# Kernel optimization log

Measured on AMD Instinct MI355X. Metric: run time of the kernel, lower is better.

## Reference

```python
import jax, jax.numpy as jnp
import numpy as np
import math

D_MODEL = 2048
K = 64
W = 512              # window_size
STRIDE = W // 2      # = 256
EMA_ALPHA = 0.9
N_RETRIEVE = 8
EPS = 1e-12


def _build_cheby(k, w):
    # cheby_mat[k, n] = cos(k * arccos(t_n)), t_n = cos(pi*(2n+1)/(2w))
    ns = np.arange(w, dtype=np.float64)
    t = np.cos(np.pi * (2 * ns + 1) / (2 * w))
    ks = np.arange(k, dtype=np.float64)
    return jnp.asarray(np.cos(ks[:, None] * np.arccos(t)[None, :]), dtype=jnp.float32)


def setup_inputs() -> dict:
    key = jax.random.key(0)
    ks = jax.random.split(key, 5)
    B, S = 2, 8192
    scan_out = jax.random.normal(ks[0], (B, S, D_MODEL), dtype=jnp.float32)
    buf = jax.random.normal(ks[1], (W, D_MODEL), dtype=jnp.float32)  # pre-filled circular buffer
    # unit-modulus random-phase complex roles: r_k[d] = exp(i*theta)
    phases = jax.random.uniform(ks[2], (K, D_MODEL), dtype=jnp.float32) * (2.0 * math.pi)
    roles_real = jnp.cos(phases)
    roles_imag = jnp.sin(phases)
    w_bands = 1.0 / (jnp.arange(K, dtype=jnp.float32) + 1.0)  # w_init = 1/(k+1)
    retrieve_proj_w = jax.random.normal(ks[3], (D_MODEL, D_MODEL), dtype=jnp.float32) * 0.02
    inject_gate = jnp.zeros((1,), dtype=jnp.float32)
    cheby_mat = _build_cheby(K, W)
    return dict(scan_out=scan_out, buf=buf, roles_real=roles_real, roles_imag=roles_imag,
                w_bands=w_bands, retrieve_proj_w=retrieve_proj_w, inject_gate=inject_gate,
                cheby_mat=cheby_mat)


def reference(scan_out, buf, roles_real, roles_imag, w_bands, retrieve_proj_w, inject_gate, cheby_mat):
    S = scan_out.shape[1]
    h_mean = scan_out.mean(axis=0)                      # [S, D] batch-mean like torch code
    n_chunks = S // STRIDE
    chunks = h_mean.reshape(n_chunks, STRIDE, D_MODEL)  # each chunk triggers one bind

    init = (buf, jnp.int32(0),
            jnp.zeros((K, D_MODEL), jnp.float32),   # c_past
            jnp.zeros((D_MODEL,), jnp.float32),     # V_mem_real
            jnp.zeros((D_MODEL,), jnp.float32),     # V_mem_imag
            jnp.zeros((K,), jnp.float32),           # _coeff_norms (EMA)
            jnp.zeros((K,), jnp.float32))           # spectral_delta

    def step(carry, chunk):
        b, pos, c_past, vr, vi, cnorms, _ = carry
        # circular-buffer write of `stride` tokens starting at pos
        b = jax.lax.dynamic_update_slice(b, chunk, (pos, 0))
        pos = (pos + STRIDE) % W
        order = (jnp.arange(W, dtype=jnp.int32) + pos) % W   # oldest-first reorder
        data = b[order]                                      # [W, D]
        # Chebyshev coefficients: c = (2/W) * cheby_mat @ data, c0 halved
        coeffs = (2.0 / W) * (cheby_mat @ data)              # [K, D]
        coeffs = coeffs.at[0].multiply(0.5)
        # HRR-normalized bind into holographic memory via EMA
        norms = jnp.maximum(jnp.linalg.norm(coeffs, axis=-1, keepdims=True), EPS)
        cn = coeffs / norms
        cnorms = EMA_ALPHA * cnorms + (1.0 - EMA_ALPHA) * norms[:, 0]
        vr = EMA_ALPHA * vr + (1.0 - EMA_ALPHA) * (cn * roles_real).sum(axis=0)
        vi = EMA_ALPHA * vi + (1.0 - EMA_ALPHA) * (cn * roles_imag).sum(axis=0)
        # spectral delta vs previous window's coefficients
        delta = jnp.linalg.norm(coeffs - c_past, axis=-1)    # [K]
        return (b, pos, coeffs, vr, vi, cnorms, delta), None

    (b, pos, c_now, vr, vi, cnorms, delta), _ = jax.lax.scan(step, init, chunks)

    # retrieve: unbind top-J bands by spectral delta, denormalize, weight, project
    _, top = jax.lax.top_k(delta, N_RETRIEVE)                # [J]
    rr = roles_real[top]
    ri = roles_imag[top]
    retrieved = (vr[None, :] * rr + vi[None, :] * ri) * jnp.maximum(cnorms[top], EPS)[:, None]  # [J, D]
    weights = jax.nn.softplus(w_bands[top])                  # [J]
    ctx = (weights[:, None] * retrieved).sum(axis=0)         # [D]
    out = (ctx @ retrieve_proj_w.T) * jax.nn.sigmoid(inject_gate[0])  # [D]
    return out, delta, vr, vi
```

## Files before the change

kernel.cpp:

```cpp
#include <hip/hip_runtime.h>
#include <math.h>

#define D_MODEL 2048
#define KB_ 64
#define NCHUNK 32

typedef __bf16 bf16;
typedef __attribute__((ext_vector_type(8))) __bf16 bf16x8;
typedef __attribute__((ext_vector_type(4))) __bf16 bf16x4;
typedef __attribute__((ext_vector_type(4))) float f32x4;

#define OFF_COEFFS 0
#define OFF_NSQ    (32 * 64 * 2048)
#define OFF_NORMS  (OFF_NSQ + 32 * 64 * 32)
#define OFF_PARTR  (OFF_NORMS + 2048)
#define OFF_PARTI  (OFF_PARTR + 32 * 2048)
#define OFF_CTX    (OFF_PARTI + 32 * 2048)
#define OFF_CHEB2  (OFF_CTX + 2048)

__global__ __launch_bounds__(256) void k0_prep(
    const float* __restrict__ cheby, bf16* __restrict__ cheb2)
{
  int flat = blockIdx.x * 256 + threadIdx.x;
  cheb2[flat] = (bf16)cheby[flat];
}

__global__ __launch_bounds__(256) void k1_mfma(
    const float* __restrict__ scan, const float* __restrict__ buf,
    const bf16* __restrict__ cheb2, float* __restrict__ coeffs,
    float* __restrict__ nsq_part)
{
  __shared__ bf16 Bs[64 * 72];

  const int t = threadIdx.x;
  const int dt = blockIdx.x;
  const int c  = blockIdx.y;
  const int w = t >> 6, lane = t & 63;
  const int quad = lane >> 4, r16 = lane & 15;
  const int d0 = dt * 64;
  const int n0 = (t >> 4) * 4;
  const int d4 = (t & 15) * 4;
  const float* scan1 = scan + 8192 * 2048;

  f32x4 acc[4];
#pragma unroll
  for (int tn = 0; tn < 4; ++tn) acc[tn] = (f32x4){0.f, 0.f, 0.f, 0.f};

  for (int nb = 0; nb < 8; ++nb) {
    const bf16* abase = cheb2 + (w * 16 + r16) * 512 + nb * 64 + quad * 8;
    bf16x8 a0 = *(const bf16x8*)(abase);
    bf16x8 a1 = *(const bf16x8*)(abase + 32);

    float vv[4][4];
    if (c == 0 && nb < 4) {
      const float* bp = buf + (256 + nb * 64 + n0) * 2048 + d0 + d4;
#pragma unroll
      for (int i = 0; i < 4; ++i) {
        float4 v = *(const float4*)(bp + i * 2048);
        vv[i][0] = v.x; vv[i][1] = v.y; vv[i][2] = v.z; vv[i][3] = v.w;
      }
    } else {
      int gbase = (c * 256 - 256 + nb * 64 + n0) * 2048 + d0 + d4;
#pragma unroll
      for (int i = 0; i < 4; ++i) {
        float4 a = *(const float4*)(scan + gbase + i * 2048);
        float4 b = *(const float4*)(scan1 + gbase + i * 2048);
        vv[i][0] = 0.5f * (a.x + b.x); vv[i][1] = 0.5f * (a.y + b.y);
        vv[i][2] = 0.5f * (a.z + b.z); vv[i][3] = 0.5f * (a.w + b.w);
      }
    }
    __syncthreads();
#pragma unroll
    for (int x = 0; x < 4; ++x) {
      bf16x4 e = {(bf16)vv[0][x], (bf16)vv[1][x], (bf16)vv[2][x], (bf16)vv[3][x]};
      *(bf16x4*)(Bs + (d4 + x) * 72 + n0) = e;
    }
    __syncthreads();

#pragma unroll
    for (int ks = 0; ks < 2; ++ks) {
      bf16x8 a = ks ? a1 : a0;
#pragma unroll
      for (int tn = 0; tn < 4; ++tn) {
        bf16x8 bfr = *(const bf16x8*)(Bs + (tn * 16 + r16) * 72 + ks * 32 + quad * 8);
        acc[tn] = __builtin_amdgcn_mfma_f32_16x16x32_bf16(a, bfr, acc[tn], 0, 0, 0);
      }
    }
  }

  const float scale = 2.0f / 512.0f;
  float sq[4] = {0.f, 0.f, 0.f, 0.f};
#pragma unroll
  for (int tn = 0; tn < 4; ++tn) {
#pragma unroll
    for (int rr = 0; rr < 4; ++rr) {
      int band = w * 16 + quad * 4 + rr;
      float sc = (band == 0) ? scale * 0.5f : scale;
      float v = acc[tn][rr] * sc;
      coeffs[(c * 64 + band) * 2048 + d0 + tn * 16 + r16] = v;
      sq[rr] += v * v;
    }
  }
#pragma unroll
  for (int off = 8; off > 0; off >>= 1) {
#pragma unroll
    for (int rr = 0; rr < 4; ++rr) sq[rr] += __shfl_down(sq[rr], off);
  }
  if (r16 == 0) {
#pragma unroll
    for (int rr = 0; rr < 4; ++rr)
      nsq_part[(c * 64 + w * 16 + quad * 4 + rr) * 32 + dt] = sq[rr];
  }
}

__global__ __launch_bounds__(256) void kd_delta(
    const float* __restrict__ coeffs, float* __restrict__ dout)
{
  const int k = blockIdx.x, tid = threadIdx.x;
  const float* p1 = coeffs + (31 * 64 + k) * 2048;
  const float* p0 = coeffs + (30 * 64 + k) * 2048;
  float s = 0.f;
#pragma unroll
  for (int i = 0; i < 2; ++i) {
    float4 a = *(const float4*)(p1 + tid * 4 + i * 1024);
    float4 b = *(const float4*)(p0 + tid * 4 + i * 1024);
    float x = a.x - b.x, y = a.y - b.y, z = a.z - b.z, ww = a.w - b.w;
    s += x * x + y * y + z * z + ww * ww;
  }
  for (int o = 32; o > 0; o >>= 1) s += __shfl_down(s, o, 64);
  __shared__ float red[4];
  if ((tid & 63) == 0) red[tid >> 6] = s;
  __syncthreads();
  if (tid == 0) dout[D_MODEL + k] = sqrtf(red[0] + red[1] + red[2] + red[3]);
}

__global__ __launch_bounds__(256) void k3_bind(
    const float* __restrict__ coeffs, const float* __restrict__ nsq_part,
    const float* __restrict__ rr, const float* __restrict__ ri,
    float* __restrict__ part_r, float* __restrict__ part_i,
    float* __restrict__ norms)
{
  __shared__ float inv_s[64];
  const int tid = threadIdx.x;
  const int c = blockIdx.y;
  if (tid < 64) {
    float s = 0.f;
#pragma unroll
    for (int dt = 0; dt < 32; ++dt) s += nsq_part[(c * 64 + tid) * 32 + dt];
    float nrm = fmaxf(sqrtf(s), 1e-12f);
    inv_s[tid] = 1.0f / nrm;
    if (blockIdx.x == 0) norms[c * 64 + tid] = nrm;
  }
  __syncthreads();
  const int d4 = (blockIdx.x * 256 + tid) * 4;
  const float wc = 0.1f * powf(0.9f, (float)(31 - c));
  float4 ar = make_float4(0.f, 0.f, 0.f, 0.f);
  float4 ai = make_float4(0.f, 0.f, 0.f, 0.f);
  for (int k = 0; k < KB_; ++k) {
    float4 cf = *(const float4*)(coeffs + (c * 64 + k) * 2048 + d4);
    float inv = inv_s[k];
    float4 r = *(const float4*)(rr + k * D_MODEL + d4);
    float4 im = *(const float4*)(ri + k * D_MODEL + d4);
    float cx = cf.x * inv, cy = cf.y * inv, cz = cf.z * inv, cw = cf.w * inv;
    ar.x += cx * r.x; ar.y += cy * r.y; ar.z += cz * r.z; ar.w += cw * r.w;
    ai.x += cx * im.x; ai.y += cy * im.y; ai.z += cz * im.z; ai.w += cw * im.w;
  }
  *(float4*)(part_r + c * D_MODEL + d4) =
      make_float4(wc * ar.x, wc * ar.y, wc * ar.z, wc * ar.w);
  *(float4*)(part_i + c * D_MODEL + d4) =
      make_float4(wc * ai.x, wc * ai.y, wc * ai.z, wc * ai.w);
}

__global__ __launch_bounds__(256) void k4_ctx(
    const float* __restrict__ norms, const float* __restrict__ part_r,
    const float* __restrict__ part_i, const float* __restrict__ rr,
    const float* __restrict__ ri, const float* __restrict__ wbands,
    float* __restrict__ dout, float* __restrict__ ctx)
{
  __shared__ float cn_s[64];
  __shared__ int top_s[8];
  __shared__ float wgt_s[8];
  const int tid = threadIdx.x;
  const int d = blockIdx.x * 256 + tid;
  if (tid < 64) {
    float s = 0.f;
    for (int c = 0; c < NCHUNK; ++c) s = 0.9f * s + 0.1f * norms[c * 64 + tid];
    cn_s[tid] = fmaxf(s, 1e-12f);
  }
  __syncthreads();
  if (tid == 0) {
    unsigned long long taken = 0ULL;
    for (int jj = 0; jj < 8; ++jj) {
      float best = -1.f;
      int bi = 0;
      for (int k = 0; k < 64; ++k) {
        float dv = dout[D_MODEL + k];
        if (!((taken >> k) & 1ULL) && dv > best) { best = dv; bi = k; }
      }
      taken |= (1ULL << bi);
      top_s[jj] = bi;
      wgt_s[jj] = log1pf(expf(wbands[bi]));
    }
  }
  __syncthreads();
  float sr = 0.f, si = 0.f;
  for (int c = 0; c < NCHUNK; ++c) {
    sr += part_r[c * D_MODEL + d];
    si += part_i[c * D_MODEL + d];
  }
  dout[D_MODEL + KB_ + d] = sr;
  dout[D_MODEL + KB_ + D_MODEL + d] = si;
  float cx = 0.f;
#pragma unroll
  for (int jj = 0; jj < 8; ++jj) {
    int k = top_s[jj];
    cx += wgt_s[jj] * (sr * rr[k * D_MODEL + d] + si * ri[k * D_MODEL + d]) * cn_s[k];
  }
  ctx[d] = cx;
}

__global__ __launch_bounds__(256) void k5b_gemv(
    const float* __restrict__ Wp, const float* __restrict__ ctx,
    const float* __restrict__ gate, float* __restrict__ dout)
{
  const int tid = threadIdx.x;
  const int lane = tid & 63;
  const int w = tid >> 6;
  const int row = blockIdx.x * 4 + w;
  const float* p = Wp + row * D_MODEL;
  float s = 0.f;
#pragma unroll
  for (int i = 0; i < 8; ++i) {
    int e = lane * 4 + i * 256;
    float4 wv = *(const float4*)(p + e);
    float4 cv = *(const float4*)(ctx + e);
    s += wv.x * cv.x + wv.y * cv.y + wv.z * cv.z + wv.w * cv.w;
  }
  for (int o = 32; o > 0; o >>= 1) s += __shfl_down(s, o, 64);
  if (lane == 0) {
    float sig = 1.f / (1.f + expf(-gate[0]));
    dout[row] = s * sig;
  }
}

extern "C" void kernel_launch(void* const* d_in, const int* in_sizes, int n_in,
                              void* d_out, int out_size, void* d_ws, size_t ws_size,
                              hipStream_t stream) {
  const float* scan  = (const float*)d_in[0];
  const float* buf   = (const float*)d_in[1];
  const float* rr    = (const float*)d_in[2];
  const float* ri    = (const float*)d_in[3];
  const float* wb    = (const float*)d_in[4];
  const float* Wp    = (const float*)d_in[5];
  const float* gate  = (const float*)d_in[6];
  const float* cheby = (const float*)d_in[7];
  float* out = (float*)d_out;
  float* ws = (float*)d_ws;

  float* coeffs   = ws + OFF_COEFFS;
  float* nsq_part = ws + OFF_NSQ;
  float* norms    = ws + OFF_NORMS;
  float* part_r   = ws + OFF_PARTR;
  float* part_i   = ws + OFF_PARTI;
  float* ctx      = ws + OFF_CTX;
  bf16*  cheb2    = (bf16*)(ws + OFF_CHEB2);

  k0_prep<<<128, 256, 0, stream>>>(cheby, cheb2);
  k1_mfma<<<dim3(32, 32), 256, 0, stream>>>(scan, buf, cheb2, coeffs, nsq_part);
  kd_delta<<<64, 256, 0, stream>>>(coeffs, out);
  k3_bind<<<dim3(2, NCHUNK), 256, 0, stream>>>(coeffs, nsq_part, rr, ri,
                                               part_r, part_i, norms);
  k4_ctx<<<8, 256, 0, stream>>>(norms, part_r, part_i, rr, ri, wb, out, ctx);
  k5b_gemv<<<512, 256, 0, stream>>>(Wp, ctx, gate, out);
}
```

Baseline: 279.4 us.

## Precompute batch-mean bf16 activations in prep kernel and atomically accumulate bind results

```diff
diff --git a/kernel.cpp b/kernel.cpp
--- a/kernel.cpp
+++ b/kernel.cpp
@@ -13,20 +13,47 @@
 #define OFF_COEFFS 0
 #define OFF_NSQ    (32 * 64 * 2048)
 #define OFF_NORMS  (OFF_NSQ + 32 * 64 * 32)
-#define OFF_PARTR  (OFF_NORMS + 2048)
-#define OFF_PARTI  (OFF_PARTR + 32 * 2048)
-#define OFF_CTX    (OFF_PARTI + 32 * 2048)
+#define OFF_VR     (OFF_NORMS + 2048)
+#define OFF_VI     (OFF_VR + 2048)
+#define OFF_CTX    (OFF_VI + 2048)
 #define OFF_CHEB2  (OFF_CTX + 2048)
+#define OFF_HM     (OFF_CHEB2 + 16384)
 
 __global__ __launch_bounds__(256) void k0_prep(
-    const float* __restrict__ cheby, bf16* __restrict__ cheb2)
-{
-  int flat = blockIdx.x * 256 + threadIdx.x;
-  cheb2[flat] = (bf16)cheby[flat];
+    const float* __restrict__ scan, const float* __restrict__ cheby,
+    bf16* __restrict__ hm, bf16* __restrict__ cheb2, float* __restrict__ vzero)
+{
+  const int b = blockIdx.x;
+  const int t = threadIdx.x;
+  if (b < 8192) {
+    const float* p0 = scan + b * 2048 + t * 8;
+    const float* p1 = p0 + 8192 * 2048;
+    float4 a0 = *(const float4*)(p0);
+    float4 a1 = *(const float4*)(p0 + 4);
+    float4 b0 = *(const float4*)(p1);
+    float4 b1 = *(const float4*)(p1 + 4);
+    bf16x8 e = {(bf16)(0.5f * (a0.x + b0.x)), (bf16)(0.5f * (a0.y + b0.y)),
+                (bf16)(0.5f * (a0.z + b0.z)), (bf16)(0.5f * (a0.w + b0.w)),
+                (bf16)(0.5f * (a1.x + b1.x)), (bf16)(0.5f * (a1.y + b1.y)),
+                (bf16)(0.5f * (a1.z + b1.z)), (bf16)(0.5f * (a1.w + b1.w))};
+    *(bf16x8*)(hm + b * 2048 + t * 8) = e;
+  } else if (b < 8208) {
+    int idx = (b - 8192) * 2048 + t * 8;
+    float4 c0 = *(const float4*)(cheby + idx);
+    float4 c1 = *(const float4*)(cheby + idx + 4);
+    bf16x8 e = {(bf16)c0.x, (bf16)c0.y, (bf16)c0.z, (bf16)c0.w,
+                (bf16)c1.x, (bf16)c1.y, (bf16)c1.z, (bf16)c1.w};
+    *(bf16x8*)(cheb2 + idx) = e;
+  } else {
+    float4 z = make_float4(0.f, 0.f, 0.f, 0.f);
+#pragma unroll
+    for (int i = 0; i < 4; ++i)
+      *(float4*)(vzero + t * 16 + i * 4) = z;
+  }
 }
 
 __global__ __launch_bounds__(256) void k1_mfma(
-    const float* __restrict__ scan, const float* __restrict__ buf,
+    const bf16* __restrict__ hm, const float* __restrict__ buf,
     const bf16* __restrict__ cheb2, float* __restrict__ coeffs,
     float* __restrict__ nsq_part)
 {
@@ -40,7 +67,6 @@
   const int d0 = dt * 64;
   const int n0 = (t >> 4) * 4;
   const int d4 = (t & 15) * 4;
-  const float* scan1 = scan + 8192 * 2048;
 
   f32x4 acc[4];
 #pragma unroll
@@ -51,28 +77,24 @@
     bf16x8 a0 = *(const bf16x8*)(abase);
     bf16x8 a1 = *(const bf16x8*)(abase + 32);
 
-    float vv[4][4];
+    bf16x4 rowv[4];
     if (c == 0 && nb < 4) {
       const float* bp = buf + (256 + nb * 64 + n0) * 2048 + d0 + d4;
 #pragma unroll
       for (int i = 0; i < 4; ++i) {
         float4 v = *(const float4*)(bp + i * 2048);
-        vv[i][0] = v.x; vv[i][1] = v.y; vv[i][2] = v.z; vv[i][3] = v.w;
+        rowv[i] = (bf16x4){(bf16)v.x, (bf16)v.y, (bf16)v.z, (bf16)v.w};
       }
     } else {
-      int gbase = (c * 256 - 256 + nb * 64 + n0) * 2048 + d0 + d4;
-#pragma unroll
-      for (int i = 0; i < 4; ++i) {
-        float4 a = *(const float4*)(scan + gbase + i * 2048);
-        float4 b = *(const float4*)(scan1 + gbase + i * 2048);
-        vv[i][0] = 0.5f * (a.x + b.x); vv[i][1] = 0.5f * (a.y + b.y);
-        vv[i][2] = 0.5f * (a.z + b.z); vv[i][3] = 0.5f * (a.w + b.w);
-      }
+      const bf16* hp = hm + (c * 256 - 256 + nb * 64 + n0) * 2048 + d0 + d4;
+#pragma unroll
+      for (int i = 0; i < 4; ++i)
+        rowv[i] = *(const bf16x4*)(hp + i * 2048);
     }
     __syncthreads();
 #pragma unroll
     for (int x = 0; x < 4; ++x) {
-      bf16x4 e = {(bf16)vv[0][x], (bf16)vv[1][x], (bf16)vv[2][x], (bf16)vv[3][x]};
+      bf16x4 e = {rowv[0][x], rowv[1][x], rowv[2][x], rowv[3][x]};
       *(bf16x4*)(Bs + (d4 + x) * 72 + n0) = e;
     }
     __syncthreads();
@@ -137,7 +159,7 @@
 __global__ __launch_bounds__(256) void k3_bind(
     const float* __restrict__ coeffs, const float* __restrict__ nsq_part,
     const float* __restrict__ rr, const float* __restrict__ ri,
-    float* __restrict__ part_r, float* __restrict__ part_i,
+    float* __restrict__ vr, float* __restrict__ vi,
     float* __restrict__ norms)
 {
   __shared__ float inv_s[64];
@@ -152,28 +174,22 @@
     if (blockIdx.x == 0) norms[c * 64 + tid] = nrm;
   }
   __syncthreads();
-  const int d4 = (blockIdx.x * 256 + tid) * 4;
+  const int d = blockIdx.x * 256 + tid;
   const float wc = 0.1f * powf(0.9f, (float)(31 - c));
-  float4 ar = make_float4(0.f, 0.f, 0.f, 0.f);
-  float4 ai = make_float4(0.f, 0.f, 0.f, 0.f);
+  float ar = 0.f, ai = 0.f;
+#pragma unroll 8
   for (int k = 0; k < KB_; ++k) {
-    float4 cf = *(const float4*)(coeffs + (c * 64 + k) * 2048 + d4);
-    float inv = inv_s[k];
-    float4 r = *(const float4*)(rr + k * D_MODEL + d4);
-    float4 im = *(const float4*)(ri + k * D_MODEL + d4);
-    float cx = cf.x * inv, cy = cf.y * inv, cz = cf.z * inv, cw = cf.w * inv;
-    ar.x += cx * r.x; ar.y += cy * r.y; ar.z += cz * r.z; ar.w += cw * r.w;
-    ai.x += cx * im.x; ai.y += cy * im.y; ai.z += cz * im.z; ai.w += cw * im.w;
-  }
-  *(float4*)(part_r + c * D_MODEL + d4) =
-      make_float4(wc * ar.x, wc * ar.y, wc * ar.z, wc * ar.w);
-  *(float4*)(part_i + c * D_MODEL + d4) =
-      make_float4(wc * ai.x, wc * ai.y, wc * ai.z, wc * ai.w);
+    float cf = coeffs[(c * 64 + k) * 2048 + d] * inv_s[k];
+    ar += cf * rr[k * D_MODEL + d];
+    ai += cf * ri[k * D_MODEL + d];
+  }
+  atomicAdd(&vr[d], wc * ar);
+  atomicAdd(&vi[d], wc * ai);
 }
 
 __global__ __launch_bounds__(256) void k4_ctx(
-    const float* __restrict__ norms, const float* __restrict__ part_r,
-    const float* __restrict__ part_i, const float* __restrict__ rr,
+    const float* __restrict__ norms, const float* __restrict__ vr,
+    const float* __restrict__ vi, const float* __restrict__ rr,
     const float* __restrict__ ri, const float* __restrict__ wbands,
     float* __restrict__ dout, float* __restrict__ ctx)
 {
@@ -203,11 +219,8 @@
     }
   }
   __syncthreads();
-  float sr = 0.f, si = 0.f;
-  for (int c = 0; c < NCHUNK; ++c) {
-    sr += part_r[c * D_MODEL + d];
-    si += part_i[c * D_MODEL + d];
-  }
+  float sr = vr[d];
+  float si = vi[d];
   dout[D_MODEL + KB_ + d] = sr;
   dout[D_MODEL + KB_ + D_MODEL + d] = si;
   float cx = 0.f;
@@ -260,16 +273,17 @@
   float* coeffs   = ws + OFF_COEFFS;
   float* nsq_part = ws + OFF_NSQ;
   float* norms    = ws + OFF_NORMS;
-  float* part_r   = ws + OFF_PARTR;
-  float* part_i   = ws + OFF_PARTI;
+  float* vr       = ws + OFF_VR;
+  float* vi       = ws + OFF_VI;
   float* ctx      = ws + OFF_CTX;
   bf16*  cheb2    = (bf16*)(ws + OFF_CHEB2);
-
-  k0_prep<<<128, 256, 0, stream>>>(cheby, cheb2);
-  k1_mfma<<<dim3(32, 32), 256, 0, stream>>>(scan, buf, cheb2, coeffs, nsq_part);
+  bf16*  hm       = (bf16*)(ws + OFF_HM);
+
+  k0_prep<<<8209, 256, 0, stream>>>(scan, cheby, hm, cheb2, vr);
+  k1_mfma<<<dim3(32, 32), 256, 0, stream>>>(hm, buf, cheb2, coeffs, nsq_part);
   kd_delta<<<64, 256, 0, stream>>>(coeffs, out);
-  k3_bind<<<dim3(2, NCHUNK), 256, 0, stream>>>(coeffs, nsq_part, rr, ri,
-                                               part_r, part_i, norms);
-  k4_ctx<<<8, 256, 0, stream>>>(norms, part_r, part_i, rr, ri, wb, out, ctx);
+  k3_bind<<<dim3(8, NCHUNK), 256, 0, stream>>>(coeffs, nsq_part, rr, ri,
+                                               vr, vi, norms);
+  k4_ctx<<<8, 256, 0, stream>>>(norms, vr, vi, rr, ri, wb, out, ctx);
   k5b_gemv<<<512, 256, 0, stream>>>(Wp, ctx, gate, out);
 }
```

After: 278.0 us. About the same (-0.5%).
